# Kernel optimization log

Hardware: AMD Instinct MI355X
Metric: run time of the kernel (lower is better)

The kernel has to match this reference:

```python
import jax, jax.numpy as jnp
import numpy as np
from jax import lax

B_, L_, EMB, VOCAB, NL, NH, CH = 4, 2048, 256, 256, 2, 8, 64
D_INNER = 2 * EMB          # expand=2
D_STATE = EMB              # d_state=emb_dim per source
D_CONV = 4
CONV_DIM = D_INNER + 2 * D_STATE
D_PROJ = 2 * D_INNER + 2 * D_STATE + NH
OUT_DIM = 256
EPS = 1e-5


def rms_norm(x, w):
    return x * lax.rsqrt(jnp.mean(x * x, axis=-1, keepdims=True) + EPS) * w


def segsum(a):
    # a: [..., T] -> [..., T, T] with entry (i,j) = sum a[j+1..i], -inf above diag
    T = a.shape[-1]
    cs = jnp.cumsum(a, axis=-1)
    seg = cs[..., :, None] - cs[..., None, :]
    mask = jnp.tril(jnp.ones((T, T), bool))
    return jnp.where(mask, seg, -jnp.inf)


def ssd(x, A, Bm, Cm, chunk):
    # x: [b,l,h,p], A: [b,l,h], Bm/Cm: [b,l,n] (ngroups=1, broadcast over heads)
    b, l, h, p = x.shape
    c = l // chunk
    x = x.reshape(b, c, chunk, h, p)
    A = A.reshape(b, c, chunk, h).transpose(0, 3, 1, 2)  # b h c l
    Bm = Bm.reshape(b, c, chunk, -1)
    Cm = Cm.reshape(b, c, chunk, -1)
    A_cs = jnp.cumsum(A, axis=-1)                        # b h c l
    L = jnp.exp(segsum(A))                               # b h c l l
    Y_diag = jnp.einsum("bcln,bcsn,bhcls,bcshp->bclhp", Cm, Bm, L, x)
    decay_states = jnp.exp(A_cs[..., -1:] - A_cs)        # b h c l
    states = jnp.einsum("bcln,bhcl,bclhp->bchpn", Bm, decay_states, x)
    states = jnp.concatenate([jnp.zeros_like(states[:, :1]), states], axis=1)  # b c+1 h p n
    decay_chunk = jnp.exp(segsum(jnp.pad(A_cs[:, :, :, -1], ((0, 0), (0, 0), (1, 0)))))  # b h c+1 c+1
    new_states = jnp.einsum("bhzc,bchpn->bzhpn", decay_chunk, states)
    states = new_states[:, :-1]                          # b c h p n
    Y_off = jnp.einsum("bcln,bchpn,bhcl->bclhp", Cm, states, jnp.exp(A_cs))
    return (Y_diag + Y_off).reshape(b, l, h, p)


def mamba2_block(u, in_proj_w, conv_w, conv_b, dt_bias, A_log, D, gnorm_w, outp_w):
    b, l, _ = u.shape
    zxbcdt = u @ in_proj_w                               # [b,l,D_PROJ]
    z = zxbcdt[..., :D_INNER]
    xBC = zxbcdt[..., D_INNER:D_INNER + CONV_DIM]
    dt = jax.nn.softplus(zxbcdt[..., -NH:] + dt_bias)    # [b,l,h]
    # causal depthwise conv1d, kernel 4
    xc = lax.conv_general_dilated(
        xBC.transpose(0, 2, 1), conv_w[:, None, :], (1,), [(D_CONV - 1, 0)],
        feature_group_count=CONV_DIM, dimension_numbers=("NCH", "OIH", "NCH"))
    xBC = jax.nn.silu(xc.transpose(0, 2, 1) + conv_b)
    xh = xBC[..., :D_INNER].reshape(b, l, NH, -1)        # [b,l,h,p]
    Bm = xBC[..., D_INNER:D_INNER + D_STATE]
    Cm = xBC[..., D_INNER + D_STATE:]
    A = -jnp.exp(A_log)                                  # [h]
    y = ssd(xh * dt[..., None], A * dt, Bm, Cm, CH)
    y = y + xh * D[:, None]
    y = y.reshape(b, l, D_INNER)
    y = rms_norm(y * jax.nn.silu(z), gnorm_w)
    return y @ outp_w


def _forward(idx, emb, in_proj_w, conv_w, conv_b, dt_bias, A_log, D,
             gnorm_w, outp_w, norm_w, normf_w, head_w):
    h = emb[idx]
    for i in range(NL):
        y = mamba2_block(rms_norm(h, norm_w[i]), in_proj_w[i], conv_w[i], conv_b[i],
                         dt_bias[i], A_log[i], D[i], gnorm_w[i], outp_w[i])
        h = y + h
    h = rms_norm(h, normf_w)
    return h @ head_w


def setup_inputs() -> dict:
    key = jax.random.key(0)
    ks = jax.random.split(key, 13)
    s = 0.02
    return {
        "x": jax.random.uniform(ks[0], (B_, L_, 1), jnp.float32),
        "emb": jax.random.normal(ks[1], (VOCAB, EMB)) * s,
        "in_proj_w": jax.random.normal(ks[2], (NL, EMB, D_PROJ)) * s,
        "conv_w": jax.random.normal(ks[3], (NL, CONV_DIM, D_CONV)) * 0.2,
        "conv_b": jax.random.normal(ks[4], (NL, CONV_DIM)) * s,
        "dt_bias": jax.random.normal(ks[5], (NL, NH)) * 0.1,
        "A_log": jnp.log(jax.random.uniform(ks[6], (NL, NH), minval=0.5, maxval=8.0)),
        "D": jax.random.normal(ks[7], (NL, NH)) * 0.5,
        "gnorm_w": 1.0 + jax.random.normal(ks[8], (NL, D_INNER)) * s,
        "outp_w": jax.random.normal(ks[9], (NL, D_INNER, EMB)) * s,
        "norm_w": 1.0 + jax.random.normal(ks[10], (NL, EMB)) * s,
        "normf_w": 1.0 + jax.random.normal(ks[11], (EMB,)) * s,
        "head_w": jax.random.normal(ks[12], (EMB, OUT_DIM)) * s,
    }


def reference(x, emb, in_proj_w, conv_w, conv_b, dt_bias, A_log, D,
              gnorm_w, outp_w, norm_w, normf_w, head_w):
    idx = jnp.clip(((VOCAB - 1) * x).astype(jnp.int32).squeeze(-1), 0, VOCAB - 1)
    return _forward(idx, emb, in_proj_w, conv_w, conv_b, dt_bias, A_log, D,
                    gnorm_w, outp_w, norm_w, normf_w, head_w)
```

## Files before the change

kernel.cpp:

```cpp
#include <hip/hip_runtime.h>
#include <cstddef>

#define NB 4
#define LSEQ 2048
#define BL (NB*LSEQ)
#define EMBD 256
#define DPROJ 1544
#define ZSTR 1600
#define DIN 512
#define DSTATE 256
#define CONVD 1024
#define NHD 8
#define PD 64
#define NC 32
#define NLAY 2
#define EPS 1e-5f

typedef __bf16 bf16x8 __attribute__((ext_vector_type(8)));
typedef float f32x4 __attribute__((ext_vector_type(4)));
typedef unsigned short u16;

__device__ float g_h [(size_t)BL*EMBD];
__device__ u16   g_ub[(size_t)BL*EMBD];
__device__ float g_zx[(size_t)BL*ZSTR];
__device__ u16   g_xbcb[(size_t)BL*CONVD];
__device__ float g_dt[(size_t)BL*NHD];
__device__ float g_acs[(size_t)NB*NHD*LSEQ];
__device__ float g_dAl[(size_t)NB*NHD*NC];
__device__ float g_y [(size_t)BL*DIN];
__device__ u16   g_yb[(size_t)BL*DIN];
__device__ u16   g_Sb[(size_t)NB*NC*NHD*PD*DSTATE];
__device__ float g_gt[(size_t)NB*NC*64*64];
__device__ u16   g_wt1[(size_t)ZSTR*EMBD];
__device__ u16   g_wt2[(size_t)EMBD*DIN];
__device__ u16   g_wt3[(size_t)EMBD*EMBD];

__device__ inline u16 f2b(float f){
  unsigned u = __float_as_uint(f);
  return (u16)((u + 0x7fffu + ((u>>16)&1u)) >> 16);
}
__device__ inline float b2f(u16 v){
  return __uint_as_float(((unsigned)v) << 16);
}

__global__ void k_embed(const float* __restrict__ x, const float* __restrict__ emb) {
  int i = blockIdx.x*256 + threadIdx.x;
  int row = i >> 8, col = i & 255;
  int idx = (int)(255.0f * x[row]);
  idx = idx < 0 ? 0 : (idx > 255 ? 255 : idx);
  g_h[i] = emb[idx*EMBD + col];
}

__global__ void k_rmsnorm(const float* __restrict__ in, const float* __restrict__ w,
                          u16* __restrict__ out) {
  int row = blockIdx.x, t = threadIdx.x;
  float v = in[(size_t)row*EMBD + t];
  float ss = v*v;
  #pragma unroll
  for (int o=32;o>0;o>>=1) ss += __shfl_down(ss,o,64);
  __shared__ float ls[4];
  if ((t&63)==0) ls[t>>6]=ss;
  __syncthreads();
  float tot = ls[0]+ls[1]+ls[2]+ls[3];
  float r = rsqrtf(tot*(1.0f/EMBD) + EPS);
  out[(size_t)row*EMBD + t] = f2b(v*r*w[t]);
}

__global__ void k_wt(const float* __restrict__ W, u16* __restrict__ WT, int K, int N) {
  __shared__ float t[64][65];
  int n0 = blockIdx.x*64, k0 = blockIdx.y*64;
  int tid = threadIdx.x;
  #pragma unroll
  for (int e=0;e<16;e++){
    int idx = tid + e*256;
    int kk = idx>>6, nn = idx&63;
    t[kk][nn] = (n0+nn < N) ? W[(size_t)(k0+kk)*N + n0+nn] : 0.f;
  }
  __syncthreads();
  #pragma unroll
  for (int e=0;e<16;e++){
    int idx = tid + e*256;
    int nn = idx>>6, kk = idx&63;
    WT[(size_t)(n0+nn)*K + k0+kk] = f2b(t[kk][nn]);
  }
}

template<int K, bool RES>
__global__ __launch_bounds__(256) void k_mfma_gemm(
    const u16* __restrict__ A, const u16* __restrict__ WT,
    const float* __restrict__ addC, float* __restrict__ C, int nstride)
{
  __shared__ u16 sA[128*64];
  __shared__ u16 sB[64*64];
  const int tid = threadIdx.x;
  const int lane = tid & 63;
  const int w = tid >> 6;
  const int bm = blockIdx.y * 128;
  const int bn = blockIdx.x * 64;
  const int r15 = lane & 15, kg = lane >> 4;
  f32x4 acc[2][4] = {};
  for (int k0 = 0; k0 < K; k0 += 64) {
    #pragma unroll
    for (int it = 0; it < 4; ++it) {
      int ch = it*256 + tid;
      int row = ch >> 3, c16 = ch & 7;
      uint4 v = *(const uint4*)(A + (size_t)(bm+row)*K + k0 + c16*8);
      *(uint4*)(sA + row*64 + ((c16 ^ (row&7))*8)) = v;
    }
    #pragma unroll
    for (int it = 0; it < 2; ++it) {
      int ch = it*256 + tid;
      int row = ch >> 3, c16 = ch & 7;
      uint4 v = *(const uint4*)(WT + (size_t)(bn+row)*K + k0 + c16*8);
      *(uint4*)(sB + row*64 + ((c16 ^ (row&7))*8)) = v;
    }
    __syncthreads();
    #pragma unroll
    for (int ks = 0; ks < 2; ++ks) {
      bf16x8 af[2], bfr[4];
      #pragma unroll
      for (int mr = 0; mr < 2; ++mr) {
        int row = w*32 + mr*16 + r15;
        int c16 = ks*4 + kg;
        af[mr] = *(const bf16x8*)(sA + row*64 + ((c16 ^ (row&7))*8));
      }
      #pragma unroll
      for (int nr = 0; nr < 4; ++nr) {
        int row = nr*16 + r15;
        int c16 = ks*4 + kg;
        bfr[nr] = *(const bf16x8*)(sB + row*64 + ((c16 ^ (row&7))*8));
      }
      #pragma unroll
      for (int mr = 0; mr < 2; ++mr)
        #pragma unroll
        for (int nr = 0; nr < 4; ++nr)
          acc[mr][nr] = __builtin_amdgcn_mfma_f32_16x16x32_bf16(af[mr], bfr[nr], acc[mr][nr], 0, 0, 0);
    }
    __syncthreads();
  }
  #pragma unroll
  for (int mr = 0; mr < 2; ++mr)
    #pragma unroll
    for (int j = 0; j < 4; ++j) {
      int grow = bm + w*32 + mr*16 + (lane>>4)*4 + j;
      #pragma unroll
      for (int nr = 0; nr < 4; ++nr) {
        int gcol = bn + nr*16 + (lane & 15);
        float v = acc[mr][nr][j];
        if (RES) v += addC[(size_t)grow*nstride + gcol];
        C[(size_t)grow*nstride + gcol] = v;
      }
    }
}

__global__ void k_dtscan(const float* __restrict__ dtb, const float* __restrict__ alog) {
  int gid = blockIdx.x;
  int cix = gid & (NC-1), bh = gid >> 5;
  int b = bh >> 3, h = bh & 7;
  int t = threadIdx.x;
  int row = b*LSEQ + cix*64 + t;
  float v = g_zx[(size_t)row*ZSTR + 1536 + h] + dtb[h];
  float sp = (v > 20.f) ? v : log1pf(__expf(v));
  g_dt[(size_t)row*NHD + h] = sp;
  float a = -__expf(alog[h]) * sp;
  #pragma unroll
  for (int o=1;o<64;o<<=1){
    float p = __shfl_up(a,o,64);
    if (t>=o) a += p;
  }
  g_acs[(size_t)bh*LSEQ + cix*64 + t] = a;
  if (t==63) g_dAl[(size_t)bh*NC + cix] = a;
}

__global__ __launch_bounds__(256) void k_conv(const float* __restrict__ cw,
                                              const float* __restrict__ cb) {
  int r0 = blockIdx.x * 4;
  int t0 = r0 & (LSEQ-1);
  int c  = threadIdx.x * 4;
  f32x4 v[7];
  #pragma unroll
  for (int i = 0; i < 7; ++i) {
    int tr = t0 - 3 + i;
    if (tr >= 0)
      v[i] = *(const f32x4*)(&g_zx[(size_t)(r0-3+i)*ZSTR + DIN + c]);
    else
      v[i] = (f32x4){0.f,0.f,0.f,0.f};
  }
  f32x4 w0 = *(const f32x4*)(&cw[(c+0)*4]);
  f32x4 w1 = *(const f32x4*)(&cw[(c+1)*4]);
  f32x4 w2 = *(const f32x4*)(&cw[(c+2)*4]);
  f32x4 w3 = *(const f32x4*)(&cw[(c+3)*4]);
  f32x4 bi = *(const f32x4*)(&cb[c]);
  #pragma unroll
  for (int j = 0; j < 4; ++j) {
    float o[4];
    #pragma unroll
    for (int ch = 0; ch < 4; ++ch) {
      const f32x4& wv = (ch==0)?w0:(ch==1)?w1:(ch==2)?w2:w3;
      float acc = bi[ch];
      #pragma unroll
      for (int k = 0; k < 4; ++k) acc += wv[k] * v[j+k][ch];
      o[ch] = acc / (1.f + __expf(-acc));
    }
    u16 o16[4];
    #pragma unroll
    for (int ch = 0; ch < 4; ++ch) o16[ch] = f2b(o[ch]);
    *(uint2*)(&g_xbcb[(size_t)(r0+j)*CONVD + c]) = *(const uint2*)o16;
  }
}

__global__ __launch_bounds__(256) void k_gmat() {
  int bc = blockIdx.x;
  int b = bc >> 5, cix = bc & 31;
  int row0 = b*LSEQ + cix*64;
  int tid = threadIdx.x, lane = tid & 63, w = tid >> 6;
  int r15 = lane & 15, kq = lane >> 4;
  __shared__ u16 sBm[64*256];
  __shared__ u16 sCm[64*256];
  #pragma unroll
  for (int e = 0; e < 8; ++e) {
    int idx = tid + e*256;
    int row = idx >> 5, c16 = idx & 31;
    uint4 vb = *(const uint4*)(&g_xbcb[(size_t)(row0+row)*CONVD + 512 + c16*8]);
    uint4 vc = *(const uint4*)(&g_xbcb[(size_t)(row0+row)*CONVD + 768 + c16*8]);
    int sw = (c16 ^ (row&7))*8;
    *(uint4*)(&sBm[row*256 + sw]) = vb;
    *(uint4*)(&sCm[row*256 + sw]) = vc;
  }
  __syncthreads();
  int S0 = w*16;
  f32x4 acc[4] = {};
  #pragma unroll
  for (int ks = 0; ks < 8; ++ks) {
    int ch = ks*4 + kq;
    int rA = S0 + r15;
    bf16x8 af = *(const bf16x8*)(&sBm[rA*256 + ((ch ^ (rA&7))*8)]);
    #pragma unroll
    for (int lt = 0; lt < 4; ++lt) {
      int rB = lt*16 + r15;
      bf16x8 bf = *(const bf16x8*)(&sCm[rB*256 + ((ch ^ (rB&7))*8)]);
      acc[lt] = __builtin_amdgcn_mfma_f32_16x16x32_bf16(af, bf, acc[lt], 0, 0, 0);
    }
  }
  float* Gt = &g_gt[(size_t)bc*64*64];
  #pragma unroll
  for (int lt = 0; lt < 4; ++lt)
    #pragma unroll
    for (int j = 0; j < 4; ++j)
      Gt[(S0 + kq*4 + j)*64 + lt*16 + r15] = acc[lt][j];
}

__global__ __launch_bounds__(512) void k_ssd1(const float* __restrict__ Dp) {
  int g = blockIdx.x;
  int h = g & 7, bc = g >> 3;
  int b = bc >> 5, cix = bc & 31;
  int row0 = b*LSEQ + cix*64;
  int bh = b*NHD + h;
  int tid = threadIdx.x;
  int lane = tid & 63, w = tid >> 6;
  int r15 = lane & 15, kq = lane >> 4;

  __shared__ u16 sBmt[256*64];
  __shared__ u16 sXt [64*64];
  __shared__ u16 sXdt[64*64];
  __shared__ u16 sM  [64*64];
  __shared__ float sAc[64];

  {
    int l = tid & 63;
    #pragma unroll
    for (int it = 0; it < 4; ++it) {
      int nc = (tid >> 6) + it*8;
      uint4 v4 = *(const uint4*)(&g_xbcb[(size_t)(row0+l)*CONVD + 512 + nc*8]);
      const u16* hp = (const u16*)&v4;
      #pragma unroll
      for (int i = 0; i < 8; ++i) {
        int n = nc*8 + i;
        sBmt[n*64 + (((l>>3) ^ (n&7))<<3) + (l&7)] = hp[i];
      }
    }
  }
  {
    int s = tid & 63, pc = tid >> 6;
    float ac  = g_acs[(size_t)bh*LSEQ + cix*64 + s];
    float dal = g_dAl[(size_t)bh*NC + cix];
    float dtv = g_dt[(size_t)(row0+s)*NHD + h];
    float dec = __expf(dal - ac);
    if (pc == 0) sAc[s] = ac;
    uint4 v4 = *(const uint4*)(&g_xbcb[(size_t)(row0+s)*CONVD + h*64 + pc*8]);
    const u16* hp = (const u16*)&v4;
    #pragma unroll
    for (int i = 0; i < 8; ++i) {
      int p = pc*8 + i;
      float xv = b2f(hp[i]) * dtv;
      int sw = (((s>>3) ^ (p&7))<<3) + (s&7);
      sXt [p*64 + sw] = f2b(xv);
      sXdt[p*64 + sw] = f2b(xv*dec);
    }
  }
  __syncthreads();

  {
    int S0  = (w >> 1)*16;
    int L0a = ((2*w) & 3)*16, L0b = L0a + 16;
    const float* Gt = &g_gt[(size_t)bc*64*64];
    int l0 = L0a + r15, l1 = L0b + r15;
    float acl0 = sAc[l0], acl1 = sAc[l1];
    #pragma unroll
    for (int j = 0; j < 4; ++j) {
      int s_ = S0 + kq*4 + j;
      float acs_ = sAc[s_];
      float g0 = Gt[s_*64 + l0];
      float g1 = Gt[s_*64 + l1];
      float m0 = (s_ <= l0) ? g0*__expf(acl0 - acs_) : 0.f;
      float m1 = (s_ <= l1) ? g1*__expf(acl1 - acs_) : 0.f;
      sM[l0*64 + (((s_>>3) ^ (l0&7))<<3) + (s_&7)] = f2b(m0);
      sM[l1*64 + (((s_>>3) ^ (l1&7))<<3) + (s_&7)] = f2b(m1);
    }
  }
  __syncthreads();

  {
    int lt = w >> 1;
    int pt0 = (2*w) & 3;
    int L0 = lt*16, P0 = pt0*16;
    f32x4 acc0 = {}, acc1 = {};
    #pragma unroll
    for (int ks = 0; ks < 2; ++ks) {
      int ch = ks*4 + kq;
      int sw = (ch ^ (r15&7))<<3;
      bf16x8 af = *(const bf16x8*)(&sM [(L0+r15)*64 + sw]);
      bf16x8 b0 = *(const bf16x8*)(&sXt[(P0+r15)*64 + sw]);
      bf16x8 b1 = *(const bf16x8*)(&sXt[(P0+16+r15)*64 + sw]);
      acc0 = __builtin_amdgcn_mfma_f32_16x16x32_bf16(af, b0, acc0, 0, 0, 0);
      acc1 = __builtin_amdgcn_mfma_f32_16x16x32_bf16(af, b1, acc1, 0, 0, 0);
    }
    float Dv = Dp[h];
    #pragma unroll
    for (int j = 0; j < 4; ++j) {
      int l = L0 + kq*4 + j;
      int p0 = P0 + r15, p1 = p0 + 16;
      float xh0 = b2f(g_xbcb[(size_t)(row0+l)*CONVD + h*64 + p0]);
      float xh1 = b2f(g_xbcb[(size_t)(row0+l)*CONVD + h*64 + p1]);
      g_y[(size_t)(row0+l)*DIN + h*64 + p0] = acc0[j] + Dv*xh0;
      g_y[(size_t)(row0+l)*DIN + h*64 + p1] = acc1[j] + Dv*xh1;
    }
  }

  {
    int P0 = (w >> 1)*16;
    int N0 = (w & 1)*128;
    f32x4 acc[8] = {};
    #pragma unroll
    for (int ks = 0; ks < 2; ++ks) {
      int ch = ks*4 + kq;
      int sw = (ch ^ (r15&7))<<3;
      bf16x8 af = *(const bf16x8*)(&sXdt[(P0+r15)*64 + sw]);
      #pragma unroll
      for (int nt = 0; nt < 8; ++nt) {
        bf16x8 bf = *(const bf16x8*)(&sBmt[(N0+nt*16+r15)*64 + sw]);
        acc[nt] = __builtin_amdgcn_mfma_f32_16x16x32_bf16(af, bf, acc[nt], 0, 0, 0);
      }
    }
    size_t Sbase = ((size_t)(bc*NHD + h))*PD*DSTATE;
    #pragma unroll
    for (int nt = 0; nt < 8; ++nt)
      #pragma unroll
      for (int j = 0; j < 4; ++j) {
        int p = P0 + kq*4 + j;
        int n = N0 + nt*16 + r15;
        g_Sb[Sbase + (size_t)p*DSTATE + n] = f2b(acc[nt][j]);
      }
  }
}

__global__ void k_sscan() {
  int i = blockIdx.x*256 + threadIdx.x;
  int pn = i & (PD*DSTATE-1);
  int bh = i >> 14;
  int b = bh >> 3, h = bh & 7;
  float carry = 0.f;
  for (int c=0;c<NC;c++){
    size_t off = ((size_t)((b*NC+c)*NHD + h))*PD*DSTATE + pn;
    float cur = b2f(g_Sb[off]);
    g_Sb[off] = f2b(carry);
    carry = carry*__expf(g_dAl[(size_t)(b*NHD+h)*NC + c]) + cur;
  }
}

__global__ __launch_bounds__(256) void k_ssd2() {
  int g = blockIdx.x;
  int h = g & 7, bc = g >> 3;
  int b = bc >> 5, cix = bc & 31;
  int row0 = b*LSEQ + cix*64;
  int bh = b*NHD + h;
  int tid = threadIdx.x;
  int lane = tid & 63, w = tid >> 6;
  int r15 = lane & 15, kq = lane >> 4;
  __shared__ u16 sSb[64*256];
  __shared__ float sAc[64];
  size_t Sbase = ((size_t)(bc*NHD + h))*PD*DSTATE;
  #pragma unroll
  for (int it = 0; it < 8; ++it) {
    int e = tid + it*256;
    int c16 = e & 31, p = e >> 5;
    uint4 v4 = *(const uint4*)(&g_Sb[Sbase + (size_t)p*DSTATE + c16*8]);
    *(uint4*)(&sSb[p*256 + ((c16 ^ (p&7))<<3)]) = v4;
  }
  if (tid < 64) sAc[tid] = g_acs[(size_t)bh*LSEQ + cix*64 + tid];
  __syncthreads();
  int L0 = w*16;
  const u16* Ab = &g_xbcb[(size_t)(row0+L0+r15)*CONVD + 768];
  f32x4 acc[4] = {};
  #pragma unroll
  for (int ks = 0; ks < 8; ++ks) {
    int ch = ks*4 + kq;
    bf16x8 af = *(const bf16x8*)(Ab + ch*8);
    #pragma unroll
    for (int pt = 0; pt < 4; ++pt) {
      bf16x8 bf = *(const bf16x8*)(&sSb[(pt*16+r15)*256 + ((ch ^ (r15&7))<<3)]);
      acc[pt] = __builtin_amdgcn_mfma_f32_16x16x32_bf16(af, bf, acc[pt], 0, 0, 0);
    }
  }
  #pragma unroll
  for (int j = 0; j < 4; ++j) {
    int l = L0 + kq*4 + j;
    float ev = __expf(sAc[l]);
    #pragma unroll
    for (int pt = 0; pt < 4; ++pt) {
      int p = pt*16 + r15;
      g_y[(size_t)(row0+l)*DIN + h*64 + p] += ev*acc[pt][j];
    }
  }
}

__global__ void k_gated(const float* __restrict__ gw) {
  int row = blockIdx.x, t = threadIdx.x;
  float v[2]; float ss = 0.f;
  #pragma unroll
  for (int e=0;e<2;e++){
    int c = t + e*256;
    float z = g_zx[(size_t)row*ZSTR + c];
    float val = g_y[(size_t)row*DIN + c] * (z/(1.f+__expf(-z)));
    v[e]=val; ss += val*val;
  }
  #pragma unroll
  for (int o=32;o>0;o>>=1) ss += __shfl_down(ss,o,64);
  __shared__ float ls[4];
  if ((t&63)==0) ls[t>>6]=ss;
  __syncthreads();
  float tot = ls[0]+ls[1]+ls[2]+ls[3];
  float r = rsqrtf(tot*(1.f/DIN) + EPS);
  #pragma unroll
  for (int e=0;e<2;e++){
    int c = t+e*256;
    g_yb[(size_t)row*DIN + c] = f2b(v[e]*r*gw[c]);
  }
}

extern "C" void kernel_launch(void* const* d_in, const int* in_sizes, int n_in,
                              void* d_out, int out_size, void* d_ws, size_t ws_size,
                              hipStream_t stream) {
  const float* x     = (const float*)d_in[0];
  const float* emb   = (const float*)d_in[1];
  const float* inpw  = (const float*)d_in[2];
  const float* convw = (const float*)d_in[3];
  const float* convb = (const float*)d_in[4];
  const float* dtb   = (const float*)d_in[5];
  const float* alog  = (const float*)d_in[6];
  const float* Dp    = (const float*)d_in[7];
  const float* gnw   = (const float*)d_in[8];
  const float* outw  = (const float*)d_in[9];
  const float* normw = (const float*)d_in[10];
  const float* normf = (const float*)d_in[11];
  const float* headw = (const float*)d_in[12];
  float* out = (float*)d_out;
  (void)in_sizes; (void)n_in; (void)out_size; (void)d_ws; (void)ws_size;

  float *ph, *pzx;
  u16 *pub, *pyb, *pwt1, *pwt2, *pwt3;
  hipGetSymbolAddress((void**)&ph,   HIP_SYMBOL(g_h));
  hipGetSymbolAddress((void**)&pub,  HIP_SYMBOL(g_ub));
  hipGetSymbolAddress((void**)&pzx,  HIP_SYMBOL(g_zx));
  hipGetSymbolAddress((void**)&pyb,  HIP_SYMBOL(g_yb));
  hipGetSymbolAddress((void**)&pwt1, HIP_SYMBOL(g_wt1));
  hipGetSymbolAddress((void**)&pwt2, HIP_SYMBOL(g_wt2));
  hipGetSymbolAddress((void**)&pwt3, HIP_SYMBOL(g_wt3));

  k_embed<<<BL*EMBD/256, 256, 0, stream>>>(x, emb);
  for (int i=0;i<NLAY;i++){
    k_rmsnorm<<<BL, 256, 0, stream>>>(ph, normw + i*EMBD, pub);
    k_wt<<<dim3(ZSTR/64, EMBD/64), 256, 0, stream>>>(inpw + (size_t)i*EMBD*DPROJ, pwt1, EMBD, DPROJ);
    k_mfma_gemm<EMBD,false><<<dim3(ZSTR/64, BL/128), 256, 0, stream>>>(pub, pwt1, nullptr, pzx, ZSTR);
    k_dtscan<<<NB*NHD*NC, 64, 0, stream>>>(dtb + i*NHD, alog + i*NHD);
    k_conv<<<BL/4, 256, 0, stream>>>(convw + i*CONVD*4, convb + i*CONVD);
    k_gmat<<<NB*NC, 256, 0, stream>>>();
    k_ssd1<<<NB*NC*NHD, 512, 0, stream>>>(Dp + i*NHD);
    k_sscan<<<(NB*NHD*PD*DSTATE)/256, 256, 0, stream>>>();
    k_ssd2<<<NB*NC*NHD, 256, 0, stream>>>();
    k_gated<<<BL, 256, 0, stream>>>(gnw + i*DIN);
    k_wt<<<dim3(EMBD/64, DIN/64), 256, 0, stream>>>(outw + (size_t)i*DIN*EMBD, pwt2, DIN, EMBD);
    k_mfma_gemm<DIN,true><<<dim3(EMBD/64, BL/128), 256, 0, stream>>>(pyb, pwt2, ph, ph, EMBD);
  }
  k_rmsnorm<<<BL, 256, 0, stream>>>(ph, normf, pub);
  k_wt<<<dim3(EMBD/64, EMBD/64), 256, 0, stream>>>(headw, pwt3, EMBD, EMBD);
  k_mfma_gemm<EMBD,false><<<dim3(EMBD/64, BL/128), 256, 0, stream>>>(pub, pwt3, nullptr, out, EMBD);
}
```

Baseline: 363.9 us.

## Batch weight transposes, fuse embed+rmsnorm, use direct global-to-LDS loads, vectorize gating

All weight transposes for both layers and the head now run in one launch up front instead of five separate launches. The embedding lookup is fused with the first RMSNorm, and later norms are moved to the end of each layer loop. The GEMM tile loads now use global_load_lds, writing straight into LDS and skipping register staging. The gated norm kernel is vectorized to handle two rows per block with float4 loads. Together these cut launch count and load overhead, at the cost of extra weight buffer space and reliance on the LDS-direct load layout matching the swizzle.

```diff
diff --git a/kernel.cpp b/kernel.cpp
--- a/kernel.cpp
+++ b/kernel.cpp
@@ -31,8 +31,8 @@
 __device__ u16   g_yb[(size_t)BL*DIN];
 __device__ u16   g_Sb[(size_t)NB*NC*NHD*PD*DSTATE];
 __device__ float g_gt[(size_t)NB*NC*64*64];
-__device__ u16   g_wt1[(size_t)ZSTR*EMBD];
-__device__ u16   g_wt2[(size_t)EMBD*DIN];
+__device__ u16   g_wt1[(size_t)NLAY*ZSTR*EMBD];
+__device__ u16   g_wt2[(size_t)NLAY*EMBD*DIN];
 __device__ u16   g_wt3[(size_t)EMBD*EMBD];
 
 __device__ inline u16 f2b(float f){
@@ -43,12 +43,28 @@
   return __uint_as_float(((unsigned)v) << 16);
 }
 
-__global__ void k_embed(const float* __restrict__ x, const float* __restrict__ emb) {
-  int i = blockIdx.x*256 + threadIdx.x;
-  int row = i >> 8, col = i & 255;
+typedef __attribute__((address_space(1))) const unsigned int gu32;
+typedef __attribute__((address_space(3))) unsigned int lu32;
+__device__ __forceinline__ void gl_lds16(const u16* g, u16* l){
+  __builtin_amdgcn_global_load_lds((gu32*)g, (lu32*)l, 16, 0, 0);
+}
+
+__global__ void k_embedrms(const float* __restrict__ x, const float* __restrict__ emb,
+                           const float* __restrict__ w) {
+  int row = blockIdx.x, t = threadIdx.x;
   int idx = (int)(255.0f * x[row]);
   idx = idx < 0 ? 0 : (idx > 255 ? 255 : idx);
-  g_h[i] = emb[idx*EMBD + col];
+  float v = emb[idx*EMBD + t];
+  g_h[(size_t)row*EMBD + t] = v;
+  float ss = v*v;
+  #pragma unroll
+  for (int o=32;o>0;o>>=1) ss += __shfl_down(ss,o,64);
+  __shared__ float ls[4];
+  if ((t&63)==0) ls[t>>6]=ss;
+  __syncthreads();
+  float tot = ls[0]+ls[1]+ls[2]+ls[3];
+  float r = rsqrtf(tot*(1.0f/EMBD) + EPS);
+  g_ub[(size_t)row*EMBD + t] = f2b(v*r*w[t]);
 }
 
 __global__ void k_rmsnorm(const float* __restrict__ in, const float* __restrict__ w,
@@ -66,22 +82,36 @@
   out[(size_t)row*EMBD + t] = f2b(v*r*w[t]);
 }
 
-__global__ void k_wt(const float* __restrict__ W, u16* __restrict__ WT, int K, int N) {
-  __shared__ float t[64][65];
-  int n0 = blockIdx.x*64, k0 = blockIdx.y*64;
-  int tid = threadIdx.x;
+__global__ void k_wtall(const float* __restrict__ inpw, const float* __restrict__ outw,
+                        const float* __restrict__ headw) {
+  __shared__ float tb[64][65];
+  int id = blockIdx.x, tid = threadIdx.x;
+  const float* W; u16* WT; int K, N, n0, k0;
+  if (id < 200) {
+    int l = id/100, r = id%100;
+    K = EMBD; N = DPROJ; n0 = (r%25)*64; k0 = (r/25)*64;
+    W = inpw + (size_t)l*EMBD*DPROJ; WT = g_wt1 + (size_t)l*ZSTR*EMBD;
+  } else if (id < 264) {
+    int r = id-200; int l = r/32; r %= 32;
+    K = DIN; N = EMBD; n0 = (r%4)*64; k0 = (r/4)*64;
+    W = outw + (size_t)l*DIN*EMBD; WT = g_wt2 + (size_t)l*EMBD*DIN;
+  } else {
+    int r = id-264;
+    K = EMBD; N = EMBD; n0 = (r%4)*64; k0 = (r/4)*64;
+    W = headw; WT = g_wt3;
+  }
   #pragma unroll
   for (int e=0;e<16;e++){
     int idx = tid + e*256;
     int kk = idx>>6, nn = idx&63;
-    t[kk][nn] = (n0+nn < N) ? W[(size_t)(k0+kk)*N + n0+nn] : 0.f;
+    tb[kk][nn] = (n0+nn < N) ? W[(size_t)(k0+kk)*N + n0+nn] : 0.f;
   }
   __syncthreads();
   #pragma unroll
   for (int e=0;e<16;e++){
     int idx = tid + e*256;
     int nn = idx>>6, kk = idx&63;
-    WT[(size_t)(n0+nn)*K + k0+kk] = f2b(t[kk][nn]);
+    WT[(size_t)(n0+nn)*K + k0+kk] = f2b(tb[kk][nn]);
   }
 }
 
@@ -98,22 +128,29 @@
   const int bm = blockIdx.y * 128;
   const int bn = blockIdx.x * 64;
   const int r15 = lane & 15, kg = lane >> 4;
+  const int lr = lane >> 3, cs = lane & 7;
+  const u16* aSrc[4]; u16* aDst[4];
+  const u16* bSrc[2]; u16* bDst[2];
+  #pragma unroll
+  for (int it = 0; it < 4; ++it) {
+    int row = it*32 + w*8 + lr;
+    int ck = cs ^ (row & 7);
+    aSrc[it] = A + (size_t)(bm+row)*K + ck*8;
+    aDst[it] = sA + it*2048 + w*512;
+  }
+  #pragma unroll
+  for (int it = 0; it < 2; ++it) {
+    int row = it*32 + w*8 + lr;
+    int ck = cs ^ (row & 7);
+    bSrc[it] = WT + (size_t)(bn+row)*K + ck*8;
+    bDst[it] = sB + it*2048 + w*512;
+  }
   f32x4 acc[2][4] = {};
   for (int k0 = 0; k0 < K; k0 += 64) {
     #pragma unroll
-    for (int it = 0; it < 4; ++it) {
-      int ch = it*256 + tid;
-      int row = ch >> 3, c16 = ch & 7;
-      uint4 v = *(const uint4*)(A + (size_t)(bm+row)*K + k0 + c16*8);
-      *(uint4*)(sA + row*64 + ((c16 ^ (row&7))*8)) = v;
-    }
-    #pragma unroll
-    for (int it = 0; it < 2; ++it) {
-      int ch = it*256 + tid;
-      int row = ch >> 3, c16 = ch & 7;
-      uint4 v = *(const uint4*)(WT + (size_t)(bn+row)*K + k0 + c16*8);
-      *(uint4*)(sB + row*64 + ((c16 ^ (row&7))*8)) = v;
-    }
+    for (int it = 0; it < 4; ++it) gl_lds16(aSrc[it] + k0, aDst[it]);
+    #pragma unroll
+    for (int it = 0; it < 2; ++it) gl_lds16(bSrc[it] + k0, bDst[it]);
     __syncthreads();
     #pragma unroll
     for (int ks = 0; ks < 2; ++ks) {
@@ -435,27 +472,29 @@
 }
 
 __global__ void k_gated(const float* __restrict__ gw) {
-  int row = blockIdx.x, t = threadIdx.x;
-  float v[2]; float ss = 0.f;
-  #pragma unroll
-  for (int e=0;e<2;e++){
-    int c = t + e*256;
-    float z = g_zx[(size_t)row*ZSTR + c];
-    float val = g_y[(size_t)row*DIN + c] * (z/(1.f+__expf(-z)));
-    v[e]=val; ss += val*val;
+  int rl = threadIdx.x >> 7;
+  int row = blockIdx.x*2 + rl;
+  int t = threadIdx.x & 127;
+  f32x4 y4 = *(const f32x4*)(&g_y[(size_t)row*DIN + t*4]);
+  f32x4 z4 = *(const f32x4*)(&g_zx[(size_t)row*ZSTR + t*4]);
+  float v[4]; float ss = 0.f;
+  #pragma unroll
+  for (int j = 0; j < 4; ++j) {
+    float z = z4[j];
+    float val = y4[j] * (z/(1.f+__expf(-z)));
+    v[j] = val; ss += val*val;
   }
   #pragma unroll
   for (int o=32;o>0;o>>=1) ss += __shfl_down(ss,o,64);
   __shared__ float ls[4];
-  if ((t&63)==0) ls[t>>6]=ss;
-  __syncthreads();
-  float tot = ls[0]+ls[1]+ls[2]+ls[3];
+  if ((threadIdx.x&63)==0) ls[threadIdx.x>>6]=ss;
+  __syncthreads();
+  float tot = ls[rl*2] + ls[rl*2+1];
   float r = rsqrtf(tot*(1.f/DIN) + EPS);
-  #pragma unroll
-  for (int e=0;e<2;e++){
-    int c = t+e*256;
-    g_yb[(size_t)row*DIN + c] = f2b(v[e]*r*gw[c]);
-  }
+  u16 o16[4];
+  #pragma unroll
+  for (int j = 0; j < 4; ++j) o16[j] = f2b(v[j]*r*gw[t*4+j]);
+  *(uint2*)(&g_yb[(size_t)row*DIN + t*4]) = *(const uint2*)o16;
 }
 
 extern "C" void kernel_launch(void* const* d_in, const int* in_sizes, int n_in,
@@ -487,22 +526,21 @@
   hipGetSymbolAddress((void**)&pwt2, HIP_SYMBOL(g_wt2));
   hipGetSymbolAddress((void**)&pwt3, HIP_SYMBOL(g_wt3));
 
-  k_embed<<<BL*EMBD/256, 256, 0, stream>>>(x, emb);
+  k_embedrms<<<BL, 256, 0, stream>>>(x, emb, normw);
+  k_wtall<<<280, 256, 0, stream>>>(inpw, outw, headw);
   for (int i=0;i<NLAY;i++){
-    k_rmsnorm<<<BL, 256, 0, stream>>>(ph, normw + i*EMBD, pub);
-    k_wt<<<dim3(ZSTR/64, EMBD/64), 256, 0, stream>>>(inpw + (size_t)i*EMBD*DPROJ, pwt1, EMBD, DPROJ);
-    k_mfma_gemm<EMBD,false><<<dim3(ZSTR/64, BL/128), 256, 0, stream>>>(pub, pwt1, nullptr, pzx, ZSTR);
+    k_mfma_gemm<EMBD,false><<<dim3(ZSTR/64, BL/128), 256, 0, stream>>>(
+        pub, pwt1 + (size_t)i*ZSTR*EMBD, nullptr, pzx, ZSTR);
     k_dtscan<<<NB*NHD*NC, 64, 0, stream>>>(dtb + i*NHD, alog + i*NHD);
     k_conv<<<BL/4, 256, 0, stream>>>(convw + i*CONVD*4, convb + i*CONVD);
     k_gmat<<<NB*NC, 256, 0, stream>>>();
     k_ssd1<<<NB*NC*NHD, 512, 0, stream>>>(Dp + i*NHD);
     k_sscan<<<(NB*NHD*PD*DSTATE)/256, 256, 0, stream>>>();
     k_ssd2<<<NB*NC*NHD, 256, 0, stream>>>();
-    k_gated<<<BL, 256, 0, stream>>>(gnw + i*DIN);
-    k_wt<<<dim3(EMBD/64, DIN/64), 256, 0, stream>>>(outw + (size_t)i*DIN*EMBD, pwt2, DIN, EMBD);
-    k_mfma_gemm<DIN,true><<<dim3(EMBD/64, BL/128), 256, 0, stream>>>(pyb, pwt2, ph, ph, EMBD);
-  }
-  k_rmsnorm<<<BL, 256, 0, stream>>>(ph, normf, pub);
-  k_wt<<<dim3(EMBD/64, EMBD/64), 256, 0, stream>>>(headw, pwt3, EMBD, EMBD);
+    k_gated<<<BL/2, 256, 0, stream>>>(gnw + i*DIN);
+    k_mfma_gemm<DIN,true><<<dim3(EMBD/64, BL/128), 256, 0, stream>>>(
+        pyb, pwt2 + (size_t)i*EMBD*DIN, ph, ph, EMBD);
+    k_rmsnorm<<<BL, 256, 0, stream>>>(ph, (i==NLAY-1) ? normf : normw + (i+1)*EMBD, pub);
+  }
   k_mfma_gemm<EMBD,false><<<dim3(EMBD/64, BL/128), 256, 0, stream>>>(pub, pwt3, nullptr, out, EMBD);
 }
```

Measured after the change: 374.1 us. +2.8%, slower.
